# Kernel optimization log

Measured on AMD Instinct MI355X. Metric: run time of the kernel, lower is better.

Reference implementation:

```python
import jax, jax.numpy as jnp
import numpy as np

K = 32   # tokens_per_obs (hard-coded in module)
V = 512  # vocab_size

def setup_inputs() -> dict:
    key = jax.random.key(0)
    ks = jax.random.split(key, 10)
    s = 0.02  # small init scale for numerical sanity
    return {
        "x": jax.random.normal(ks[0], (4096, 512), jnp.float32),
        "enc_w1": jax.random.normal(ks[1], (512, 512), jnp.float32) * s,
        "enc_b1": jnp.zeros((512,), jnp.float32),
        "enc_w2": jax.random.normal(ks[2], (512, 16384), jnp.float32) * s,
        "enc_b2": jnp.zeros((16384,), jnp.float32),
        "codebook": jax.random.uniform(ks[3], (16384, 256), jnp.float32, -1.0 / V, 1.0 / V),
        "dec_w1": jax.random.normal(ks[4], (256, 512), jnp.float32) * s,
        "dec_b1": jnp.zeros((512,), jnp.float32),
        "dec_w2": jax.random.normal(ks[5], (512, 512), jnp.float32) * s,
        "dec_b2": jnp.zeros((512,), jnp.float32),
    }

def reference(x, enc_w1, enc_b1, enc_w2, enc_b2, codebook,
              dec_w1, dec_b1, dec_w2, dec_b2):
    b = x.shape[0]
    # encoder MLP -> logits z of shape (b, K*V)
    h = jax.nn.relu(x @ enc_w1 + enc_b1)
    z = h @ enc_w2 + enc_b2
    zl = z.reshape(b, K, V)                      # (b, K, V) per-block logits
    # categorical sample per token block
    tokens = jax.random.categorical(jax.random.key(1), zl, axis=-1)  # (b, K) int
    p = jax.nn.softmax(zl, axis=-1).reshape(b, K * V)
    oh = jax.nn.one_hot(tokens, V, dtype=p.dtype).reshape(b, K * V)
    # straight-through: forward value == one-hot, gradient flows through p
    st = p + jax.lax.stop_gradient(oh - p)
    z_q = st @ codebook                          # (b, embed_dim) = sum of K code rows
    # decoder MLP -> reconstruction
    rec = jax.nn.relu(z_q @ dec_w1 + dec_b1) @ dec_w2 + dec_b2
    return z, z_q, rec
```

## Files before the change

### kernel.cpp

```cpp
#include <hip/hip_runtime.h>
#include <hip/hip_bf16.h>
#include <math.h>
#include <stdint.h>


#define BATCH 4096
#define KTOK  32
#define VOCAB 512
#define DMODEL 512
#define ZDIM  16384
#define EDIM  256
#define MARGIN 0.03125f

typedef __attribute__((ext_vector_type(8))) short short8v;
typedef __attribute__((ext_vector_type(4))) float f32x4;

__device__ __forceinline__ uint32_t rotl32(uint32_t v, int r) {
    return (v << r) | (v >> (32 - r));
}

__device__ __forceinline__ void threefry2x32(uint32_t k0, uint32_t k1,
                                             uint32_t x0, uint32_t x1,
                                             uint32_t& y0, uint32_t& y1) {
    uint32_t ks0 = k0, ks1 = k1, ks2 = k0 ^ k1 ^ 0x1BD11BDAu;
    x0 += ks0; x1 += ks1;
#define TFR(r) { x0 += x1; x1 = rotl32(x1, r); x1 ^= x0; }
    TFR(13) TFR(15) TFR(26) TFR(6)
    x0 += ks1; x1 += ks2 + 1u;
    TFR(17) TFR(29) TFR(16) TFR(24)
    x0 += ks2; x1 += ks0 + 2u;
    TFR(13) TFR(15) TFR(26) TFR(6)
    x0 += ks0; x1 += ks1 + 3u;
    TFR(17) TFR(29) TFR(16) TFR(24)
    x0 += ks1; x1 += ks2 + 4u;
    TFR(13) TFR(15) TFR(26) TFR(6)
    x0 += ks2; x1 += ks0 + 5u;
#undef TFR
    y0 = x0; y1 = x1;
}

__device__ __forceinline__ float jax_gumbel(uint64_t e) {
    const float TINY = 1.17549435e-38f;
    uint32_t y0, y1;
    threefry2x32(0u, 1u, (uint32_t)(e >> 32), (uint32_t)(e & 0xffffffffull), y0, y1);
    uint32_t bits = y0 ^ y1;
    float u = __uint_as_float(0x3f800000u | (bits >> 9)) - 1.0f;
    u = u * 1.0f + TINY;
    u = fmaxf(TINY, u);
    return -logf(-logf(u));
}

__device__ __forceinline__ float fast_gumbel(uint32_t e32) {
    const float TINY = 1.17549435e-38f;
    const float LN2 = 0.69314718056f;
    uint32_t y0, y1;
    threefry2x32(0u, 1u, 0u, e32, y0, y1);
    uint32_t bits = y0 ^ y1;
    float f = __uint_as_float(0x3f800000u | (bits >> 9));
    float u = f - 1.0f;
    float d = 2.0f - f;
    u = fmaxf(u, TINY);
    float e_hw = -LN2 * __builtin_amdgcn_logf(u);
    float e_poly = d * fmaf(d, fmaf(d, 0.33333333f, 0.5f), 1.0f);
    float e = (d < 0.002f) ? e_poly : e_hw;
    return -LN2 * __builtin_amdgcn_logf(e);
}

__device__ __forceinline__ unsigned short f32_to_bf16_rne(float f) {
    uint32_t u = __float_as_uint(f);
    uint32_t r = (u + 0x7fffu + ((u >> 16) & 1u)) >> 16;
    return (unsigned short)r;
}

template<bool RELU>
__global__ __launch_bounds__(256)
void gemm_f32_64(const float* __restrict__ A, const float* __restrict__ B,
                 const float* __restrict__ bias, float* __restrict__ C,
                 int M, int N, int K) {
    constexpr int BK = 16;
    __shared__ __align__(16) float As[BK][68];
    __shared__ __align__(16) float Bs[BK][68];

    const int tid = threadIdx.x;
    const int tx = tid % 16;
    const int ty = tid / 16;
    const int brow = blockIdx.y * 64;
    const int bcol = blockIdx.x * 64;

    float acc[4][4] = {};

    for (int k0 = 0; k0 < K; k0 += BK) {
        {
            int r = tid >> 2, c4 = tid & 3;
            float4 v = *(const float4*)&A[(size_t)(brow + r) * K + k0 + c4 * 4];
            As[c4 * 4 + 0][r] = v.x;
            As[c4 * 4 + 1][r] = v.y;
            As[c4 * 4 + 2][r] = v.z;
            As[c4 * 4 + 3][r] = v.w;
        }
        {
            int r = tid >> 4, c4 = tid & 15;
            *(float4*)&Bs[r][c4 * 4] = *(const float4*)&B[(size_t)(k0 + r) * N + bcol + c4 * 4];
        }
        __syncthreads();

#pragma unroll
        for (int kk = 0; kk < BK; ++kk) {
            float a[4], b[4];
            *(float4*)&a[0] = *(const float4*)&As[kk][ty * 4];
            *(float4*)&b[0] = *(const float4*)&Bs[kk][tx * 4];
#pragma unroll
            for (int i = 0; i < 4; ++i)
#pragma unroll
                for (int j = 0; j < 4; ++j)
                    acc[i][j] = fmaf(a[i], b[j], acc[i][j]);
        }
        __syncthreads();
    }

#pragma unroll
    for (int i = 0; i < 4; ++i) {
        int row = brow + ty * 4 + i;
        int col = bcol + tx * 4;
        float4 v;
        v.x = acc[i][0] + bias[col + 0];
        v.y = acc[i][1] + bias[col + 1];
        v.z = acc[i][2] + bias[col + 2];
        v.w = acc[i][3] + bias[col + 3];
        if (RELU) {
            v.x = fmaxf(v.x, 0.0f); v.y = fmaxf(v.y, 0.0f);
            v.z = fmaxf(v.z, 0.0f); v.w = fmaxf(v.w, 0.0f);
        }
        *(float4*)&C[(size_t)row * N + col] = v;
    }
}

template<bool RELU>
__global__ __launch_bounds__(256)
void gemm_f32(const float* __restrict__ A, const float* __restrict__ B,
              const float* __restrict__ bias, float* __restrict__ C,
              int M, int N, int K) {
    constexpr int BM = 128, BN = 128, BK = 16, TM = 8, TN = 8;
    __shared__ __align__(16) float As[BK][BM + 4];
    __shared__ __align__(16) float Bs[BK][BN + 4];

    const int tid = threadIdx.x;
    const int tx = tid % (BN / TN);
    const int ty = tid / (BN / TN);
    const int brow = blockIdx.y * BM;
    const int bcol = blockIdx.x * BN;

    float acc[TM][TN] = {};

    for (int k0 = 0; k0 < K; k0 += BK) {
#pragma unroll
        for (int f = tid; f < BM * BK / 4; f += 256) {
            int r = f / (BK / 4);
            int c4 = f % (BK / 4);
            float4 v = *(const float4*)&A[(size_t)(brow + r) * K + k0 + c4 * 4];
            As[c4 * 4 + 0][r] = v.x;
            As[c4 * 4 + 1][r] = v.y;
            As[c4 * 4 + 2][r] = v.z;
            As[c4 * 4 + 3][r] = v.w;
        }
#pragma unroll
        for (int f = tid; f < BK * BN / 4; f += 256) {
            int r = f / (BN / 4);
            int c4 = f % (BN / 4);
            *(float4*)&Bs[r][c4 * 4] = *(const float4*)&B[(size_t)(k0 + r) * N + bcol + c4 * 4];
        }
        __syncthreads();

#pragma unroll
        for (int kk = 0; kk < BK; ++kk) {
            float a[TM], b[TN];
            *(float4*)&a[0] = *(const float4*)&As[kk][ty * TM];
            *(float4*)&a[4] = *(const float4*)&As[kk][ty * TM + 4];
            *(float4*)&b[0] = *(const float4*)&Bs[kk][tx * TN];
            *(float4*)&b[4] = *(const float4*)&Bs[kk][tx * TN + 4];
#pragma unroll
            for (int i = 0; i < TM; ++i)
#pragma unroll
                for (int j = 0; j < TN; ++j)
                    acc[i][j] = fmaf(a[i], b[j], acc[i][j]);
        }
        __syncthreads();
    }

#pragma unroll
    for (int i = 0; i < TM; ++i) {
        int row = brow + ty * TM + i;
#pragma unroll
        for (int j = 0; j < TN; j += 4) {
            int col = bcol + tx * TN + j;
            float4 v;
            v.x = acc[i][j + 0] + bias[col + 0];
            v.y = acc[i][j + 1] + bias[col + 1];
            v.z = acc[i][j + 2] + bias[col + 2];
            v.w = acc[i][j + 3] + bias[col + 3];
            if (RELU) {
                v.x = fmaxf(v.x, 0.0f); v.y = fmaxf(v.y, 0.0f);
                v.z = fmaxf(v.z, 0.0f); v.w = fmaxf(v.w, 0.0f);
            }
            *(float4*)&C[(size_t)row * N + col] = v;
        }
    }
}

__global__ __launch_bounds__(256)
void cvt_to_bf16(const float* __restrict__ src, unsigned short* __restrict__ dst,
                 int n) {
    int i = blockIdx.x * 256 + threadIdx.x;
    if (i * 4 < n) {
        float4 v = *(const float4*)&src[i * 4];
        ushort4 o;
        o.x = f32_to_bf16_rne(v.x);
        o.y = f32_to_bf16_rne(v.y);
        o.z = f32_to_bf16_rne(v.z);
        o.w = f32_to_bf16_rne(v.w);
        *(ushort4*)&dst[i * 4] = o;
    }
}

__global__ __launch_bounds__(256)
void transpose_w2(const float* __restrict__ src, unsigned short* __restrict__ dstb,
                  float* __restrict__ dstf, int R, int C, int writeF) {
    __shared__ float tile[32][33];
    const int c0 = blockIdx.x * 32, r0 = blockIdx.y * 32;
    const int tx = threadIdx.x % 32, ty = threadIdx.x / 32;
#pragma unroll
    for (int i = ty; i < 32; i += 8)
        tile[i][tx] = src[(size_t)(r0 + i) * C + c0 + tx];
    __syncthreads();
#pragma unroll
    for (int i = ty; i < 32; i += 8) {
        float v = tile[tx][i];
        size_t o = (size_t)(c0 + i) * R + r0 + tx;
        dstb[o] = f32_to_bf16_rne(v);
        if (writeF) dstf[o] = v;
    }
}

__global__ __launch_bounds__(256)
void gemm_mfma_bf16(const unsigned short* __restrict__ A,
                    const unsigned short* __restrict__ Bt,
                    const float* __restrict__ bias,
                    float* __restrict__ C,
                    int M, int N, int K) {
    constexpr int BM = 128, BN = 128, BK = 32;
    __shared__ unsigned short As[BM * BK];
    __shared__ unsigned short Bs[BN * BK];

    const int nwg = gridDim.x * gridDim.y;
    const int lid = blockIdx.y * gridDim.x + blockIdx.x;
    const int cpx = nwg >> 3;
    const int swz = (lid & 7) * cpx + (lid >> 3);
    const int bx = swz % gridDim.x;
    const int by = swz / gridDim.x;

    const int tid = threadIdx.x;
    const int wid = tid >> 6;
    const int lane = tid & 63;
    const int wr = wid >> 1, wc = wid & 1;
    const int l15 = lane & 15, lq = lane >> 4;
    const int brow = by * BM;
    const int bcol = bx * BN;

    const int g1 = tid;
    const int g2 = tid + 256;
    const size_t a1 = (size_t)(brow + (g1 >> 2)) * K + (g1 & 3) * 8;
    const size_t a2 = (size_t)(brow + (g2 >> 2)) * K + (g2 & 3) * 8;
    const size_t b1 = (size_t)(bcol + (g1 >> 2)) * K + (g1 & 3) * 8;
    const size_t b2 = (size_t)(bcol + (g2 >> 2)) * K + (g2 & 3) * 8;
    unsigned short* as_base1 = As + (size_t)wid * 64 * 8;
    unsigned short* as_base2 = As + (size_t)(256 + wid * 64) * 8;
    unsigned short* bs_base1 = Bs + (size_t)wid * 64 * 8;
    unsigned short* bs_base2 = Bs + (size_t)(256 + wid * 64) * 8;

    f32x4 acc[4][4];
#pragma unroll
    for (int m = 0; m < 4; ++m)
#pragma unroll
        for (int n = 0; n < 4; ++n) acc[m][n] = (f32x4){0.f, 0.f, 0.f, 0.f};

    for (int k0 = 0; k0 < K; k0 += BK) {
        __builtin_amdgcn_global_load_lds(
            (const __attribute__((address_space(1))) unsigned int*)(A + a1 + k0),
            (__attribute__((address_space(3))) unsigned int*)as_base1, 16, 0, 0);
        __builtin_amdgcn_global_load_lds(
            (const __attribute__((address_space(1))) unsigned int*)(A + a2 + k0),
            (__attribute__((address_space(3))) unsigned int*)as_base2, 16, 0, 0);
        __builtin_amdgcn_global_load_lds(
            (const __attribute__((address_space(1))) unsigned int*)(Bt + b1 + k0),
            (__attribute__((address_space(3))) unsigned int*)bs_base1, 16, 0, 0);
        __builtin_amdgcn_global_load_lds(
            (const __attribute__((address_space(1))) unsigned int*)(Bt + b2 + k0),
            (__attribute__((address_space(3))) unsigned int*)bs_base2, 16, 0, 0);
        __syncthreads();

        short8v af[4], bf[4];
#pragma unroll
        for (int m = 0; m < 4; ++m)
            af[m] = *(const short8v*)&As[(wr * 64 + m * 16 + l15) * BK + lq * 8];
#pragma unroll
        for (int n = 0; n < 4; ++n)
            bf[n] = *(const short8v*)&Bs[(wc * 64 + n * 16 + l15) * BK + lq * 8];
#pragma unroll
        for (int m = 0; m < 4; ++m)
#pragma unroll
            for (int n = 0; n < 4; ++n)
                acc[m][n] = __builtin_amdgcn_mfma_f32_16x16x32_bf16(
                    af[m], bf[n], acc[m][n], 0, 0, 0);
        __syncthreads();
    }

#pragma unroll
    for (int m = 0; m < 4; ++m) {
#pragma unroll
        for (int n = 0; n < 4; ++n) {
            int col = bcol + wc * 64 + n * 16 + l15;
            float bv = bias[col];
#pragma unroll
            for (int r = 0; r < 4; ++r) {
                int row = brow + wr * 64 + m * 16 + lq * 4 + r;
                C[(size_t)row * N + col] = acc[m][n][r] + bv;
            }
        }
    }
}

__global__ __launch_bounds__(256)
void sample_tokens_gap(const float* __restrict__ z, int* __restrict__ tokens,
                       float* __restrict__ s1v, int* __restrict__ amb,
                       int* __restrict__ ambCount) {
    const int wave = threadIdx.x >> 6;
    const int lane = threadIdx.x & 63;
    const uint32_t t = blockIdx.x * 4 + wave;
    const float* zr = z + (size_t)t * VOCAB;

    float s1 = -INFINITY, s2 = -INFINITY;
    int v1 = 0;
#pragma unroll
    for (int half = 0; half < 2; ++half) {
        int e0 = half * 256 + lane * 4;
        float4 zv = *(const float4*)&zr[e0];
        float zs[4] = {zv.x, zv.y, zv.z, zv.w};
#pragma unroll
        for (int j = 0; j < 4; ++j) {
            int v = e0 + j;
            float s = zs[j] + fast_gumbel(t * (uint32_t)VOCAB + v);
            if (s > s1 || (s == s1 && v < v1)) { s2 = s1; s1 = s; v1 = v; }
            else if (s > s2) s2 = s;
        }
    }
#pragma unroll
    for (int off = 32; off > 0; off >>= 1) {
        float os1 = __shfl_down(s1, off);
        int ov1 = __shfl_down(v1, off);
        float os2 = __shfl_down(s2, off);
        if (os1 > s1 || (os1 == s1 && ov1 < v1)) {
            s2 = fmaxf(s1, os2); s1 = os1; v1 = ov1;
        } else {
            s2 = fmaxf(os1, s2);
        }
    }
    if (lane == 0) {
        tokens[t] = v1;
        s1v[t] = s1;
        if (s1 - s2 < MARGIN) {
            int idx = atomicAdd(ambCount, 1);
            amb[idx] = (int)t;
        }
    }
}

__global__ __launch_bounds__(64)
void refine_tokens2(const float* __restrict__ z, const float* __restrict__ h,
                    const float* __restrict__ w2t, const float* __restrict__ eb2,
                    const int* __restrict__ amb, const int* __restrict__ ambCount,
                    const float* __restrict__ s1v, int* __restrict__ tok) {
    __shared__ float hrow[DMODEL];
    __shared__ int candv[64];
    const int cnt = *ambCount;
    const int lane = threadIdx.x;

    for (int i = blockIdx.x; i < cnt; i += gridDim.x) {
        const int t = amb[i];
        const int b = t >> 5;
        const int kb = t & 31;
        const float* zr = z + (size_t)t * VOCAB;
        const float s1 = s1v[t];

        {
            float4 hv0 = *(const float4*)&h[(size_t)b * DMODEL + lane * 8];
            float4 hv1 = *(const float4*)&h[(size_t)b * DMODEL + lane * 8 + 4];
            *(float4*)&hrow[lane * 8] = hv0;
            *(float4*)&hrow[lane * 8 + 4] = hv1;
        }

        int base = 0;
#pragma unroll
        for (int half = 0; half < 2; ++half) {
            int e0 = half * 256 + lane * 4;
            float4 zv = *(const float4*)&zr[e0];
            float zs[4] = {zv.x, zv.y, zv.z, zv.w};
#pragma unroll
            for (int j = 0; j < 4; ++j) {
                int v = e0 + j;
                float s = zs[j] + fast_gumbel((uint32_t)t * VOCAB + v);
                bool pred = (s >= s1 - MARGIN);
                unsigned long long mask = __ballot(pred);
                if (pred) {
                    int slot = base + __popcll(mask & ((1ull << lane) - 1ull));
                    if (slot < 64) candv[slot] = v;
                }
                base += __popcll(mask);
            }
        }
        __syncthreads();
        const int ncand = base < 64 ? base : 64;

        float bestE = -INFINITY;
        int bestV = VOCAB;
        if (lane < ncand) {
            const int v = candv[lane];
            const int n = kb * VOCAB + v;
            const float* wr_ = w2t + (size_t)n * DMODEL;
            float acc = 0.f;
#pragma unroll 8
            for (int k = 0; k < DMODEL; ++k)
                acc = fmaf(hrow[k], wr_[k], acc);
            bestE = acc + eb2[n] + jax_gumbel((uint64_t)t * VOCAB + v);
            bestV = v;
        }
#pragma unroll
        for (int off = 32; off > 0; off >>= 1) {
            float oe = __shfl_down(bestE, off);
            int ov = __shfl_down(bestV, off);
            if (oe > bestE || (oe == bestE && ov < bestV)) { bestE = oe; bestV = ov; }
        }
        if (lane == 0) tok[t] = bestV;
        __syncthreads();
    }
}

__global__ __launch_bounds__(64)
void refine_tokens(const float* __restrict__ z, const float* __restrict__ h,
                   const float* __restrict__ w2, const float* __restrict__ eb2,
                   const int* __restrict__ amb, const int* __restrict__ ambCount,
                   const float* __restrict__ s1v, int* __restrict__ tok) {
    const int cnt = *ambCount;
    const int lane = threadIdx.x;
    for (int i = blockIdx.x; i < cnt; i += gridDim.x) {
        const int t = amb[i];
        const int b = t >> 5;
        const int kb = t & 31;
        const float* zr = z + (size_t)t * VOCAB;
        const float s1 = s1v[t];
        float bestE = -INFINITY;
        int bestV = VOCAB;
#pragma unroll 1
        for (int r = 0; r < 8; ++r) {
            const int v = r * 64 + lane;
            const float g = jax_gumbel((uint64_t)t * VOCAB + v);
            const float sbf = zr[v] + g;
            float ex = -INFINITY;
            if (sbf >= s1 - MARGIN) {
                const float* hr = h + (size_t)b * DMODEL;
                const float* wcol = w2 + (size_t)(kb * VOCAB + v);
                float acc = 0.f;
#pragma unroll 8
                for (int k = 0; k < DMODEL; ++k)
                    acc = fmaf(hr[k], wcol[(size_t)k * ZDIM], acc);
                ex = acc + eb2[kb * VOCAB + v] + g;
            }
            if (ex > bestE || (ex == bestE && v < bestV)) { bestE = ex; bestV = v; }
        }
#pragma unroll
        for (int off = 32; off > 0; off >>= 1) {
            float oe = __shfl_down(bestE, off);
            int ov = __shfl_down(bestV, off);
            if (oe > bestE || (oe == bestE && ov < bestV)) { bestE = oe; bestV = ov; }
        }
        if (lane == 0) tok[t] = bestV;
    }
}

__global__ __launch_bounds__(256)
void sample_tokens_simple(const float* __restrict__ z, int* __restrict__ tokens) {
    const int wave = threadIdx.x >> 6;
    const int lane = threadIdx.x & 63;
    const size_t t = (size_t)blockIdx.x * 4 + wave;
    const float* zr = z + t * VOCAB;
    float zv[8];
    *(float4*)&zv[0] = *(const float4*)&zr[lane * 8];
    *(float4*)&zv[4] = *(const float4*)&zr[lane * 8 + 4];
    const uint64_t ebase = t * (uint64_t)VOCAB + (uint64_t)lane * 8;
    float best = -INFINITY;
    int bestv = 0;
#pragma unroll
    for (int j = 0; j < 8; ++j) {
        float g = jax_gumbel(ebase + j);
        float s = zv[j] + g;
        int v = lane * 8 + j;
        if (s > best || (s == best && v < bestv)) { best = s; bestv = v; }
    }
#pragma unroll
    for (int off = 32; off > 0; off >>= 1) {
        float ob = __shfl_down(best, off);
        int ov = __shfl_down(bestv, off);
        if (ob > best || (ob == best && ov < bestv)) { best = ob; bestv = ov; }
    }
    if (lane == 0) tokens[t] = bestv;
}

__global__ __launch_bounds__(64)
void zero_count(int* p) { if (threadIdx.x == 0) *p = 0; }

__global__ __launch_bounds__(256)
void gather_zq(const int* __restrict__ tokens, const float* __restrict__ codebook,
               float* __restrict__ zq) {
    const int b = blockIdx.x;
    const int d = threadIdx.x;
    float s = 0.0f;
#pragma unroll
    for (int k = 0; k < KTOK; ++k) {
        int tok = tokens[b * KTOK + k];
        s += codebook[(size_t)(k * VOCAB + tok) * EDIM + d];
    }
    zq[(size_t)b * EDIM + d] = s;
}

extern "C" void kernel_launch(void* const* d_in, const int* in_sizes, int n_in,
                              void* d_out, int out_size, void* d_ws, size_t ws_size,
                              hipStream_t stream) {
    const float* x   = (const float*)d_in[0];
    const float* ew1 = (const float*)d_in[1];
    const float* eb1 = (const float*)d_in[2];
    const float* ew2 = (const float*)d_in[3];
    const float* eb2 = (const float*)d_in[4];
    const float* cb  = (const float*)d_in[5];
    const float* dw1 = (const float*)d_in[6];
    const float* db1 = (const float*)d_in[7];
    const float* dw2 = (const float*)d_in[8];
    const float* db2 = (const float*)d_in[9];

    float* out = (float*)d_out;
    float* z   = out;
    float* zq  = out + (size_t)BATCH * ZDIM;
    float* rec = zq + (size_t)BATCH * EDIM;

    char* ws = (char*)d_ws;
    float* h    = (float*)(ws);
    float* h2   = (float*)(ws + 8388608);
    unsigned short* hb   = (unsigned short*)(ws + 16777216);
    unsigned short* w2bt = (unsigned short*)(ws + 20971520);
    float* w2t  = (float*)(ws + 37748736);
    const size_t WS_NEED1 = 39321856;
    const size_t WS_NEED2 = 37748736 + 33554432 + 1572864 + 256;
    const bool fast  = ws_size >= WS_NEED1;
    const bool fast2 = ws_size >= WS_NEED2;
    char* tail = fast2 ? (ws + 37748736 + 33554432) : (ws + 37748736);
    int*   tok  = (int*)(tail);
    float* s1v  = (float*)(tail + 524288);
    int*   amb  = (int*)(tail + 1048576);
    int*   cnt  = (int*)(tail + 1572864);

    dim3 blk(256);

    gemm_f32_64<true ><<<dim3(DMODEL / 64, BATCH / 64), blk, 0, stream>>>(
        x, ew1, eb1, h, BATCH, DMODEL, DMODEL);

    if (fast) {
        cvt_to_bf16<<<dim3(BATCH * DMODEL / 4 / 256), blk, 0, stream>>>(
            h, hb, BATCH * DMODEL);
        transpose_w2<<<dim3(ZDIM / 32, DMODEL / 32), blk, 0, stream>>>(
            ew2, w2bt, w2t, DMODEL, ZDIM, fast2 ? 1 : 0);
        gemm_mfma_bf16<<<dim3(ZDIM / 128, BATCH / 128), blk, 0, stream>>>(
            hb, w2bt, eb2, z, BATCH, ZDIM, DMODEL);
        zero_count<<<dim3(1), dim3(64), 0, stream>>>(cnt);
        sample_tokens_gap<<<dim3(BATCH * KTOK / 4), blk, 0, stream>>>(
            z, tok, s1v, amb, cnt);
        if (fast2) {
            refine_tokens2<<<dim3(4096), dim3(64), 0, stream>>>(
                z, h, w2t, eb2, amb, cnt, s1v, tok);
        } else {
            refine_tokens<<<dim3(2048), dim3(64), 0, stream>>>(
                z, h, ew2, eb2, amb, cnt, s1v, tok);
        }
    } else {
        gemm_f32<false><<<dim3(ZDIM / 128, BATCH / 128), blk, 0, stream>>>(
            h, ew2, eb2, z, BATCH, ZDIM, DMODEL);
        sample_tokens_simple<<<dim3(BATCH * KTOK / 4), blk, 0, stream>>>(z, tok);
    }

    gather_zq<<<dim3(BATCH), blk, 0, stream>>>(tok, cb, zq);

    gemm_f32_64<true ><<<dim3(DMODEL / 64, BATCH / 64), blk, 0, stream>>>(
        zq, dw1, db1, h2, BATCH, DMODEL, EDIM);
    gemm_f32_64<false><<<dim3(DMODEL / 64, BATCH / 64), blk, 0, stream>>>(
        h2, dw2, db2, rec, BATCH, DMODEL, DMODEL);
}
```

Measured before the change: 448.7 us.

## Fuse encoder GEMM with Gumbel top-2 sampling in one kernel

Replaces the separate bf16 MFMA GEMM and the sampling kernel with one kernel. Each block computes a 64x512 tile of z, which covers one vocab block per row, and adds Gumbel noise in the epilogue. It then does the top-2 reduction through shuffles and LDS, writing tokens and ambiguity flags directly. This removes the second full read of the 256MB z tensor. The cost is a different tile shape (512-thread blocks, 2x8 accumulators) and heavy threefry work in the GEMM epilogue, which may lower occupancy.

```diff
diff --git a/kernel.cpp b/kernel.cpp
--- a/kernel.cpp
+++ b/kernel.cpp
@@ -15,16 +15,12 @@
 typedef __attribute__((ext_vector_type(8))) short short8v;
 typedef __attribute__((ext_vector_type(4))) float f32x4;
 
-__device__ __forceinline__ uint32_t rotl32(uint32_t v, int r) {
-    return (v << r) | (v >> (32 - r));
-}
-
 __device__ __forceinline__ void threefry2x32(uint32_t k0, uint32_t k1,
                                              uint32_t x0, uint32_t x1,
                                              uint32_t& y0, uint32_t& y1) {
     uint32_t ks0 = k0, ks1 = k1, ks2 = k0 ^ k1 ^ 0x1BD11BDAu;
     x0 += ks0; x1 += ks1;
-#define TFR(r) { x0 += x1; x1 = rotl32(x1, r); x1 ^= x0; }
+#define TFR(r) { x0 += x1; x1 = __builtin_rotateleft32(x1, r); x1 ^= x0; }
     TFR(13) TFR(15) TFR(26) TFR(6)
     x0 += ks1; x1 += ks2 + 1u;
     TFR(17) TFR(29) TFR(16) TFR(24)
@@ -72,6 +68,28 @@
     return (unsigned short)r;
 }
 
+__device__ __forceinline__ void top2_push(float& s1, float& s2, int& v1,
+                                          float s, int v) {
+    if (s > s1 || (s == s1 && v < v1)) { s2 = s1; s1 = s; v1 = v; }
+    else s2 = fmaxf(s2, s);
+}
+__device__ __forceinline__ void top2_merge(float& s1, float& s2, int& v1,
+                                           float os1, float os2, int ov1) {
+    if (os1 > s1 || (os1 == s1 && ov1 < v1)) {
+        s2 = fmaxf(s1, os2);
+        s1 = os1; v1 = ov1;
+    } else {
+        s2 = fmaxf(s2, os1);
+    }
+}
+
+__device__ __forceinline__ void gload16(const unsigned short* src,
+                                        unsigned short* lds_base) {
+    __builtin_amdgcn_global_load_lds(
+        (const __attribute__((address_space(1))) unsigned int*)src,
+        (__attribute__((address_space(3))) unsigned int*)lds_base, 16, 0, 0);
+}
+
 template<bool RELU>
 __global__ __launch_bounds__(256)
 void gemm_f32_64(const float* __restrict__ A, const float* __restrict__ B,
@@ -241,133 +259,128 @@
     }
 }
 
-__global__ __launch_bounds__(256)
-void gemm_mfma_bf16(const unsigned short* __restrict__ A,
-                    const unsigned short* __restrict__ Bt,
-                    const float* __restrict__ bias,
-                    float* __restrict__ C,
-                    int M, int N, int K) {
-    constexpr int BM = 128, BN = 128, BK = 32;
-    __shared__ unsigned short As[BM * BK];
-    __shared__ unsigned short Bs[BN * BK];
-
-    const int nwg = gridDim.x * gridDim.y;
-    const int lid = blockIdx.y * gridDim.x + blockIdx.x;
-    const int cpx = nwg >> 3;
-    const int swz = (lid & 7) * cpx + (lid >> 3);
-    const int bx = swz % gridDim.x;
-    const int by = swz / gridDim.x;
+__global__ __launch_bounds__(512, 4)
+void gemm_fused_sample(const unsigned short* __restrict__ A,
+                       const unsigned short* __restrict__ Bt,
+                       const float* __restrict__ bias,
+                       float* __restrict__ C,
+                       int* __restrict__ tokens, float* __restrict__ s1v,
+                       int* __restrict__ amb, int* __restrict__ ambCount) {
+    __shared__ unsigned short As[4 * 64 * 8];
+    __shared__ unsigned short Bs[4 * 512 * 8];
+    __shared__ float redS1[64][4];
+    __shared__ float redS2[64][4];
+    __shared__ int   redV[64][4];
+
+    const int lid = blockIdx.x;
+    const int swz = (lid & 7) * 256 + (lid >> 3);
+    const int bx = swz >> 6;
+    const int by = swz & 63;
 
     const int tid = threadIdx.x;
     const int wid = tid >> 6;
     const int lane = tid & 63;
-    const int wr = wid >> 1, wc = wid & 1;
+    const int wr2 = wid >> 2, wc = wid & 3;
     const int l15 = lane & 15, lq = lane >> 4;
-    const int brow = by * BM;
-    const int bcol = bx * BN;
-
-    const int g1 = tid;
-    const int g2 = tid + 256;
-    const size_t a1 = (size_t)(brow + (g1 >> 2)) * K + (g1 & 3) * 8;
-    const size_t a2 = (size_t)(brow + (g2 >> 2)) * K + (g2 & 3) * 8;
-    const size_t b1 = (size_t)(bcol + (g1 >> 2)) * K + (g1 & 3) * 8;
-    const size_t b2 = (size_t)(bcol + (g2 >> 2)) * K + (g2 & 3) * 8;
-    unsigned short* as_base1 = As + (size_t)wid * 64 * 8;
-    unsigned short* as_base2 = As + (size_t)(256 + wid * 64) * 8;
-    unsigned short* bs_base1 = Bs + (size_t)wid * 64 * 8;
-    unsigned short* bs_base2 = Bs + (size_t)(256 + wid * 64) * 8;
-
-    f32x4 acc[4][4];
-#pragma unroll
-    for (int m = 0; m < 4; ++m)
-#pragma unroll
-        for (int n = 0; n < 4; ++n) acc[m][n] = (f32x4){0.f, 0.f, 0.f, 0.f};
-
-    for (int k0 = 0; k0 < K; k0 += BK) {
-        __builtin_amdgcn_global_load_lds(
-            (const __attribute__((address_space(1))) unsigned int*)(A + a1 + k0),
-            (__attribute__((address_space(3))) unsigned int*)as_base1, 16, 0, 0);
-        __builtin_amdgcn_global_load_lds(
-            (const __attribute__((address_space(1))) unsigned int*)(A + a2 + k0),
-            (__attribute__((address_space(3))) unsigned int*)as_base2, 16, 0, 0);
-        __builtin_amdgcn_global_load_lds(
-            (const __attribute__((address_space(1))) unsigned int*)(Bt + b1 + k0),
-            (__attribute__((address_space(3))) unsigned int*)bs_base1, 16, 0, 0);
-        __builtin_amdgcn_global_load_lds(
-            (const __attribute__((address_space(1))) unsigned int*)(Bt + b2 + k0),
-            (__attribute__((address_space(3))) unsigned int*)bs_base2, 16, 0, 0);
-        __syncthreads();
-
-        short8v af[4], bf[4];
-#pragma unroll
-        for (int m = 0; m < 4; ++m)
-            af[m] = *(const short8v*)&As[(wr * 64 + m * 16 + l15) * BK + lq * 8];
-#pragma unroll
-        for (int n = 0; n < 4; ++n)
-            bf[n] = *(const short8v*)&Bs[(wc * 64 + n * 16 + l15) * BK + lq * 8];
-#pragma unroll
-        for (int m = 0; m < 4; ++m)
-#pragma unroll
-            for (int n = 0; n < 4; ++n)
+    const int brow = by * 64;
+    const int bcol = bx * 512;
+
+    const unsigned short* aSrc = A + (size_t)(brow + lane) * DMODEL;
+    const unsigned short* bSrc = Bt + (size_t)(bcol + wid * 64 + lane) * DMODEL;
+
+    f32x4 acc[2][8];
+#pragma unroll
+    for (int m = 0; m < 2; ++m)
+#pragma unroll
+        for (int n = 0; n < 8; ++n) acc[m][n] = (f32x4){0.f, 0.f, 0.f, 0.f};
+
+    for (int k0 = 0; k0 < DMODEL; k0 += 32) {
+        if (wid < 4)
+            gload16(aSrc + k0 + wid * 8, As + wid * 512);
+#pragma unroll
+        for (int kq = 0; kq < 4; ++kq)
+            gload16(bSrc + k0 + kq * 8, Bs + kq * 4096 + wid * 512);
+        __syncthreads();
+
+        short8v af[2], bf[8];
+#pragma unroll
+        for (int m = 0; m < 2; ++m)
+            af[m] = *(const short8v*)&As[lq * 512 + (wr2 * 32 + m * 16 + l15) * 8];
+#pragma unroll
+        for (int n = 0; n < 8; ++n)
+            bf[n] = *(const short8v*)&Bs[lq * 4096 + (wc * 128 + n * 16 + l15) * 8];
+#pragma unroll
+        for (int m = 0; m < 2; ++m)
+#pragma unroll
+            for (int n = 0; n < 8; ++n)
                 acc[m][n] = __builtin_amdgcn_mfma_f32_16x16x32_bf16(
                     af[m], bf[n], acc[m][n], 0, 0, 0);
         __syncthreads();
     }
 
-#pragma unroll
-    for (int m = 0; m < 4; ++m) {
-#pragma unroll
-        for (int n = 0; n < 4; ++n) {
-            int col = bcol + wc * 64 + n * 16 + l15;
-            float bv = bias[col];
+    float s1[2][4], s2[2][4];
+    int v1[2][4];
+#pragma unroll
+    for (int m = 0; m < 2; ++m)
+#pragma unroll
+        for (int r = 0; r < 4; ++r) {
+            s1[m][r] = -INFINITY; s2[m][r] = -INFINITY; v1[m][r] = VOCAB;
+        }
+
+#pragma unroll
+    for (int m = 0; m < 2; ++m) {
+#pragma unroll
+        for (int n = 0; n < 8; ++n) {
+            const int col = wc * 128 + n * 16 + l15;
+            const float bv = bias[bcol + col];
 #pragma unroll
             for (int r = 0; r < 4; ++r) {
-                int row = brow + wr * 64 + m * 16 + lq * 4 + r;
-                C[(size_t)row * N + col] = acc[m][n][r] + bv;
+                const int row = wr2 * 32 + m * 16 + lq * 4 + r;
+                const float val = acc[m][n][r] + bv;
+                C[(size_t)(brow + row) * ZDIM + bcol + col] = val;
+                const uint32_t t = (uint32_t)(brow + row) * KTOK + bx;
+                const float g = fast_gumbel(t * (uint32_t)VOCAB + (uint32_t)col);
+                top2_push(s1[m][r], s2[m][r], v1[m][r], val + g, col);
             }
         }
     }
-}
-
-__global__ __launch_bounds__(256)
-void sample_tokens_gap(const float* __restrict__ z, int* __restrict__ tokens,
-                       float* __restrict__ s1v, int* __restrict__ amb,
-                       int* __restrict__ ambCount) {
-    const int wave = threadIdx.x >> 6;
-    const int lane = threadIdx.x & 63;
-    const uint32_t t = blockIdx.x * 4 + wave;
-    const float* zr = z + (size_t)t * VOCAB;
-
-    float s1 = -INFINITY, s2 = -INFINITY;
-    int v1 = 0;
-#pragma unroll
-    for (int half = 0; half < 2; ++half) {
-        int e0 = half * 256 + lane * 4;
-        float4 zv = *(const float4*)&zr[e0];
-        float zs[4] = {zv.x, zv.y, zv.z, zv.w};
-#pragma unroll
-        for (int j = 0; j < 4; ++j) {
-            int v = e0 + j;
-            float s = zs[j] + fast_gumbel(t * (uint32_t)VOCAB + v);
-            if (s > s1 || (s == s1 && v < v1)) { s2 = s1; s1 = s; v1 = v; }
-            else if (s > s2) s2 = s;
-        }
-    }
-#pragma unroll
-    for (int off = 32; off > 0; off >>= 1) {
-        float os1 = __shfl_down(s1, off);
-        int ov1 = __shfl_down(v1, off);
-        float os2 = __shfl_down(s2, off);
-        if (os1 > s1 || (os1 == s1 && ov1 < v1)) {
-            s2 = fmaxf(s1, os2); s1 = os1; v1 = ov1;
-        } else {
-            s2 = fmaxf(os1, s2);
-        }
-    }
-    if (lane == 0) {
-        tokens[t] = v1;
-        s1v[t] = s1;
-        if (s1 - s2 < MARGIN) {
+
+#pragma unroll
+    for (int off = 1; off < 16; off <<= 1) {
+#pragma unroll
+        for (int m = 0; m < 2; ++m)
+#pragma unroll
+            for (int r = 0; r < 4; ++r) {
+                float os1 = __shfl_xor(s1[m][r], off);
+                float os2 = __shfl_xor(s2[m][r], off);
+                int   ov1 = __shfl_xor(v1[m][r], off);
+                top2_merge(s1[m][r], s2[m][r], v1[m][r], os1, os2, ov1);
+            }
+    }
+    if (l15 == 0) {
+#pragma unroll
+        for (int m = 0; m < 2; ++m)
+#pragma unroll
+            for (int r = 0; r < 4; ++r) {
+                const int row = wr2 * 32 + m * 16 + lq * 4 + r;
+                redS1[row][wc] = s1[m][r];
+                redS2[row][wc] = s2[m][r];
+                redV[row][wc]  = v1[m][r];
+            }
+    }
+    __syncthreads();
+
+    if (tid < 64) {
+        const int row = tid;
+        float S1 = -INFINITY, S2 = -INFINITY;
+        int V1 = VOCAB;
+#pragma unroll
+        for (int w = 0; w < 4; ++w)
+            top2_merge(S1, S2, V1, redS1[row][w], redS2[row][w], redV[row][w]);
+        const uint32_t t = (uint32_t)(brow + row) * KTOK + bx;
+        tokens[t] = V1;
+        s1v[t] = S1;
+        if (S1 - S2 < MARGIN) {
             int idx = atomicAdd(ambCount, 1);
             amb[idx] = (int)t;
         }
@@ -576,11 +589,9 @@
             h, hb, BATCH * DMODEL);
         transpose_w2<<<dim3(ZDIM / 32, DMODEL / 32), blk, 0, stream>>>(
             ew2, w2bt, w2t, DMODEL, ZDIM, fast2 ? 1 : 0);
-        gemm_mfma_bf16<<<dim3(ZDIM / 128, BATCH / 128), blk, 0, stream>>>(
-            hb, w2bt, eb2, z, BATCH, ZDIM, DMODEL);
         zero_count<<<dim3(1), dim3(64), 0, stream>>>(cnt);
-        sample_tokens_gap<<<dim3(BATCH * KTOK / 4), blk, 0, stream>>>(
-            z, tok, s1v, amb, cnt);
+        gemm_fused_sample<<<dim3(2048), dim3(512), 0, stream>>>(
+            hb, w2bt, eb2, z, tok, s1v, amb, cnt);
         if (fast2) {
             refine_tokens2<<<dim3(4096), dim3(64), 0, stream>>>(
                 z, h, w2t, eb2, amb, cnt, s1v, tok);
```

New measurement: 501.4 us. 1.12x slower.

## Fuse gumbel top-2 sampling into MFMA GEMM epilogue and bf16 cast into GEMM1

Applied to the files above, without the earlier changes.

The bf16 GEMM epilogue now adds the Gumbel noise and computes per-row top-2 partials over each 64-column slice. The partials are merged by a small kernel that compacts ambiguous tokens using a wave ballot and one atomic per wave. This avoids re-reading the 256MB logits tensor in a separate sampling pass. The first GEMM also writes a bf16 copy of h directly, which removes the conversion kernel. In exchange the GEMM epilogue carries much more ALU work from the hash and log evaluations, and the workspace requirement grows.

```diff
diff --git a/kernel.cpp b/kernel.cpp
--- a/kernel.cpp
+++ b/kernel.cpp
@@ -15,16 +15,12 @@
 typedef __attribute__((ext_vector_type(8))) short short8v;
 typedef __attribute__((ext_vector_type(4))) float f32x4;
 
-__device__ __forceinline__ uint32_t rotl32(uint32_t v, int r) {
-    return (v << r) | (v >> (32 - r));
-}
-
 __device__ __forceinline__ void threefry2x32(uint32_t k0, uint32_t k1,
                                              uint32_t x0, uint32_t x1,
                                              uint32_t& y0, uint32_t& y1) {
     uint32_t ks0 = k0, ks1 = k1, ks2 = k0 ^ k1 ^ 0x1BD11BDAu;
     x0 += ks0; x1 += ks1;
-#define TFR(r) { x0 += x1; x1 = rotl32(x1, r); x1 ^= x0; }
+#define TFR(r) { x0 += x1; x1 = __builtin_rotateleft32(x1, r); x1 ^= x0; }
     TFR(13) TFR(15) TFR(26) TFR(6)
     x0 += ks1; x1 += ks2 + 1u;
     TFR(17) TFR(29) TFR(16) TFR(24)
@@ -72,10 +68,33 @@
     return (unsigned short)r;
 }
 
+__device__ __forceinline__ void top2_push(float& s1, float& s2, int& v1,
+                                          float s, int v) {
+    if (s > s1 || (s == s1 && v < v1)) { s2 = s1; s1 = s; v1 = v; }
+    else s2 = fmaxf(s2, s);
+}
+__device__ __forceinline__ void top2_merge(float& s1, float& s2, int& v1,
+                                           float os1, float os2, int ov1) {
+    if (os1 > s1 || (os1 == s1 && ov1 < v1)) {
+        s2 = fmaxf(s1, os2);
+        s1 = os1; v1 = ov1;
+    } else {
+        s2 = fmaxf(s2, os1);
+    }
+}
+
+__device__ __forceinline__ void gload16(const unsigned short* src,
+                                        unsigned short* lds_base) {
+    __builtin_amdgcn_global_load_lds(
+        (const __attribute__((address_space(1))) unsigned int*)src,
+        (__attribute__((address_space(3))) unsigned int*)lds_base, 16, 0, 0);
+}
+
 template<bool RELU>
 __global__ __launch_bounds__(256)
 void gemm_f32_64(const float* __restrict__ A, const float* __restrict__ B,
                  const float* __restrict__ bias, float* __restrict__ C,
+                 unsigned short* __restrict__ Cb,
                  int M, int N, int K) {
     constexpr int BK = 16;
     __shared__ __align__(16) float As[BK][68];
@@ -132,6 +151,14 @@
             v.z = fmaxf(v.z, 0.0f); v.w = fmaxf(v.w, 0.0f);
         }
         *(float4*)&C[(size_t)row * N + col] = v;
+        if (Cb) {
+            ushort4 o;
+            o.x = f32_to_bf16_rne(v.x);
+            o.y = f32_to_bf16_rne(v.y);
+            o.z = f32_to_bf16_rne(v.z);
+            o.w = f32_to_bf16_rne(v.w);
+            *(ushort4*)&Cb[(size_t)row * N + col] = o;
+        }
     }
 }
 
@@ -208,21 +235,6 @@
 }
 
 __global__ __launch_bounds__(256)
-void cvt_to_bf16(const float* __restrict__ src, unsigned short* __restrict__ dst,
-                 int n) {
-    int i = blockIdx.x * 256 + threadIdx.x;
-    if (i * 4 < n) {
-        float4 v = *(const float4*)&src[i * 4];
-        ushort4 o;
-        o.x = f32_to_bf16_rne(v.x);
-        o.y = f32_to_bf16_rne(v.y);
-        o.z = f32_to_bf16_rne(v.z);
-        o.w = f32_to_bf16_rne(v.w);
-        *(ushort4*)&dst[i * 4] = o;
-    }
-}
-
-__global__ __launch_bounds__(256)
 void transpose_w2(const float* __restrict__ src, unsigned short* __restrict__ dstb,
                   float* __restrict__ dstf, int R, int C, int writeF) {
     __shared__ float tile[32][33];
@@ -242,11 +254,12 @@
 }
 
 __global__ __launch_bounds__(256)
-void gemm_mfma_bf16(const unsigned short* __restrict__ A,
-                    const unsigned short* __restrict__ Bt,
-                    const float* __restrict__ bias,
-                    float* __restrict__ C,
-                    int M, int N, int K) {
+void gemm_mfma_fused(const unsigned short* __restrict__ A,
+                     const unsigned short* __restrict__ Bt,
+                     const float* __restrict__ bias,
+                     float* __restrict__ C,
+                     float4* __restrict__ part,
+                     int M, int N, int K) {
     constexpr int BM = 128, BN = 128, BK = 32;
     __shared__ unsigned short As[BM * BK];
     __shared__ unsigned short Bs[BN * BK];
@@ -284,18 +297,10 @@
         for (int n = 0; n < 4; ++n) acc[m][n] = (f32x4){0.f, 0.f, 0.f, 0.f};
 
     for (int k0 = 0; k0 < K; k0 += BK) {
-        __builtin_amdgcn_global_load_lds(
-            (const __attribute__((address_space(1))) unsigned int*)(A + a1 + k0),
-            (__attribute__((address_space(3))) unsigned int*)as_base1, 16, 0, 0);
-        __builtin_amdgcn_global_load_lds(
-            (const __attribute__((address_space(1))) unsigned int*)(A + a2 + k0),
-            (__attribute__((address_space(3))) unsigned int*)as_base2, 16, 0, 0);
-        __builtin_amdgcn_global_load_lds(
-            (const __attribute__((address_space(1))) unsigned int*)(Bt + b1 + k0),
-            (__attribute__((address_space(3))) unsigned int*)bs_base1, 16, 0, 0);
-        __builtin_amdgcn_global_load_lds(
-            (const __attribute__((address_space(1))) unsigned int*)(Bt + b2 + k0),
-            (__attribute__((address_space(3))) unsigned int*)bs_base2, 16, 0, 0);
+        gload16(A + a1 + k0, as_base1);
+        gload16(A + a2 + k0, as_base2);
+        gload16(Bt + b1 + k0, bs_base1);
+        gload16(Bt + b2 + k0, bs_base2);
         __syncthreads();
 
         short8v af[4], bf[4];
@@ -314,63 +319,80 @@
         __syncthreads();
     }
 
+    const int kb = bcol >> 9;
+    const int hx = ((bcol & 511) >> 6) + wc;
+
 #pragma unroll
     for (int m = 0; m < 4; ++m) {
+        float s1[4], s2[4];
+        int v1[4];
+#pragma unroll
+        for (int r = 0; r < 4; ++r) {
+            s1[r] = -INFINITY; s2[r] = -INFINITY; v1[r] = VOCAB;
+        }
 #pragma unroll
         for (int n = 0; n < 4; ++n) {
-            int col = bcol + wc * 64 + n * 16 + l15;
-            float bv = bias[col];
+            const int col = bcol + wc * 64 + n * 16 + l15;
+            const int vglob = col & 511;
+            const float bv = bias[col];
 #pragma unroll
             for (int r = 0; r < 4; ++r) {
-                int row = brow + wr * 64 + m * 16 + lq * 4 + r;
-                C[(size_t)row * N + col] = acc[m][n][r] + bv;
+                const int row = brow + wr * 64 + m * 16 + lq * 4 + r;
+                const float val = acc[m][n][r] + bv;
+                C[(size_t)row * N + col] = val;
+                const uint32_t t = (uint32_t)row * KTOK + kb;
+                const float g = fast_gumbel(t * (uint32_t)VOCAB + (uint32_t)vglob);
+                top2_push(s1[r], s2[r], v1[r], val + g, vglob);
             }
         }
-    }
-}
-
-__global__ __launch_bounds__(256)
-void sample_tokens_gap(const float* __restrict__ z, int* __restrict__ tokens,
-                       float* __restrict__ s1v, int* __restrict__ amb,
-                       int* __restrict__ ambCount) {
-    const int wave = threadIdx.x >> 6;
+#pragma unroll
+        for (int off = 1; off < 16; off <<= 1) {
+#pragma unroll
+            for (int r = 0; r < 4; ++r) {
+                float os1 = __shfl_xor(s1[r], off);
+                float os2 = __shfl_xor(s2[r], off);
+                int   ov1 = __shfl_xor(v1[r], off);
+                top2_merge(s1[r], s2[r], v1[r], os1, os2, ov1);
+            }
+        }
+        if (l15 == 0) {
+#pragma unroll
+            for (int r = 0; r < 4; ++r) {
+                const int row = brow + wr * 64 + m * 16 + lq * 4 + r;
+                const uint32_t t = (uint32_t)row * KTOK + kb;
+                float4 p;
+                p.x = s1[r]; p.y = s2[r];
+                p.z = __int_as_float(v1[r]); p.w = 0.f;
+                part[(size_t)t * 8 + hx] = p;
+            }
+        }
+    }
+}
+
+__global__ __launch_bounds__(256)
+void merge_sample(const float4* __restrict__ part, int* __restrict__ tokens,
+                  float* __restrict__ s1v, int* __restrict__ amb,
+                  int* __restrict__ ambCount) {
+    const int t = blockIdx.x * 256 + threadIdx.x;
     const int lane = threadIdx.x & 63;
-    const uint32_t t = blockIdx.x * 4 + wave;
-    const float* zr = z + (size_t)t * VOCAB;
-
-    float s1 = -INFINITY, s2 = -INFINITY;
-    int v1 = 0;
-#pragma unroll
-    for (int half = 0; half < 2; ++half) {
-        int e0 = half * 256 + lane * 4;
-        float4 zv = *(const float4*)&zr[e0];
-        float zs[4] = {zv.x, zv.y, zv.z, zv.w};
-#pragma unroll
-        for (int j = 0; j < 4; ++j) {
-            int v = e0 + j;
-            float s = zs[j] + fast_gumbel(t * (uint32_t)VOCAB + v);
-            if (s > s1 || (s == s1 && v < v1)) { s2 = s1; s1 = s; v1 = v; }
-            else if (s > s2) s2 = s;
-        }
-    }
-#pragma unroll
-    for (int off = 32; off > 0; off >>= 1) {
-        float os1 = __shfl_down(s1, off);
-        int ov1 = __shfl_down(v1, off);
-        float os2 = __shfl_down(s2, off);
-        if (os1 > s1 || (os1 == s1 && ov1 < v1)) {
-            s2 = fmaxf(s1, os2); s1 = os1; v1 = ov1;
-        } else {
-            s2 = fmaxf(os1, s2);
-        }
-    }
-    if (lane == 0) {
-        tokens[t] = v1;
-        s1v[t] = s1;
-        if (s1 - s2 < MARGIN) {
-            int idx = atomicAdd(ambCount, 1);
-            amb[idx] = (int)t;
-        }
+    float S1 = -INFINITY, S2 = -INFINITY;
+    int V1 = VOCAB;
+#pragma unroll
+    for (int hx = 0; hx < 8; ++hx) {
+        float4 p = part[(size_t)t * 8 + hx];
+        top2_merge(S1, S2, V1, p.x, p.y, __float_as_int(p.z));
+    }
+    tokens[t] = V1;
+    s1v[t] = S1;
+    const bool pred = (S1 - S2 < MARGIN);
+    unsigned long long mask = __ballot(pred);
+    if (pred) {
+        const int leader = (int)__ffsll((long long)mask) - 1;
+        int base = 0;
+        if (lane == leader) base = atomicAdd(ambCount, __popcll(mask));
+        base = __shfl(base, leader);
+        const int slot = base + __popcll(mask & ((1ull << lane) - 1ull));
+        amb[slot] = t;
     }
 }
 
@@ -441,48 +463,6 @@
         }
         if (lane == 0) tok[t] = bestV;
         __syncthreads();
-    }
-}
-
-__global__ __launch_bounds__(64)
-void refine_tokens(const float* __restrict__ z, const float* __restrict__ h,
-                   const float* __restrict__ w2, const float* __restrict__ eb2,
-                   const int* __restrict__ amb, const int* __restrict__ ambCount,
-                   const float* __restrict__ s1v, int* __restrict__ tok) {
-    const int cnt = *ambCount;
-    const int lane = threadIdx.x;
-    for (int i = blockIdx.x; i < cnt; i += gridDim.x) {
-        const int t = amb[i];
-        const int b = t >> 5;
-        const int kb = t & 31;
-        const float* zr = z + (size_t)t * VOCAB;
-        const float s1 = s1v[t];
-        float bestE = -INFINITY;
-        int bestV = VOCAB;
-#pragma unroll 1
-        for (int r = 0; r < 8; ++r) {
-            const int v = r * 64 + lane;
-            const float g = jax_gumbel((uint64_t)t * VOCAB + v);
-            const float sbf = zr[v] + g;
-            float ex = -INFINITY;
-            if (sbf >= s1 - MARGIN) {
-                const float* hr = h + (size_t)b * DMODEL;
-                const float* wcol = w2 + (size_t)(kb * VOCAB + v);
-                float acc = 0.f;
-#pragma unroll 8
-                for (int k = 0; k < DMODEL; ++k)
-                    acc = fmaf(hr[k], wcol[(size_t)k * ZDIM], acc);
-                ex = acc + eb2[kb * VOCAB + v] + g;
-            }
-            if (ex > bestE || (ex == bestE && v < bestV)) { bestE = ex; bestV = v; }
-        }
-#pragma unroll
-        for (int off = 32; off > 0; off >>= 1) {
-            float oe = __shfl_down(bestE, off);
-            int ov = __shfl_down(bestV, off);
-            if (oe > bestE || (oe == bestE && ov < bestV)) { bestE = oe; bestV = ov; }
-        }
-        if (lane == 0) tok[t] = bestV;
     }
 }
 
@@ -556,11 +536,11 @@
     unsigned short* hb   = (unsigned short*)(ws + 16777216);
     unsigned short* w2bt = (unsigned short*)(ws + 20971520);
     float* w2t  = (float*)(ws + 37748736);
-    const size_t WS_NEED1 = 39321856;
-    const size_t WS_NEED2 = 37748736 + 33554432 + 1572864 + 256;
-    const bool fast  = ws_size >= WS_NEED1;
+    float4* part = (float4*)(ws + 71303168);
+    char* tail = ws + 88080384;
+    const size_t WS_NEED2 = 88080384 + 1572864 + 256;
     const bool fast2 = ws_size >= WS_NEED2;
-    char* tail = fast2 ? (ws + 37748736 + 33554432) : (ws + 37748736);
+    if (!fast2) tail = ws + 16777216;
     int*   tok  = (int*)(tail);
     float* s1v  = (float*)(tail + 524288);
     int*   amb  = (int*)(tail + 1048576);
@@ -569,25 +549,19 @@
     dim3 blk(256);
 
     gemm_f32_64<true ><<<dim3(DMODEL / 64, BATCH / 64), blk, 0, stream>>>(
-        x, ew1, eb1, h, BATCH, DMODEL, DMODEL);
-
-    if (fast) {
-        cvt_to_bf16<<<dim3(BATCH * DMODEL / 4 / 256), blk, 0, stream>>>(
-            h, hb, BATCH * DMODEL);
+        x, ew1, eb1, h, fast2 ? hb : (unsigned short*)nullptr,
+        BATCH, DMODEL, DMODEL);
+
+    if (fast2) {
         transpose_w2<<<dim3(ZDIM / 32, DMODEL / 32), blk, 0, stream>>>(
-            ew2, w2bt, w2t, DMODEL, ZDIM, fast2 ? 1 : 0);
-        gemm_mfma_bf16<<<dim3(ZDIM / 128, BATCH / 128), blk, 0, stream>>>(
-            hb, w2bt, eb2, z, BATCH, ZDIM, DMODEL);
+            ew2, w2bt, w2t, DMODEL, ZDIM, 1);
         zero_count<<<dim3(1), dim3(64), 0, stream>>>(cnt);
-        sample_tokens_gap<<<dim3(BATCH * KTOK / 4), blk, 0, stream>>>(
-            z, tok, s1v, amb, cnt);
-        if (fast2) {
-            refine_tokens2<<<dim3(4096), dim3(64), 0, stream>>>(
-                z, h, w2t, eb2, amb, cnt, s1v, tok);
-        } else {
-            refine_tokens<<<dim3(2048), dim3(64), 0, stream>>>(
-                z, h, ew2, eb2, amb, cnt, s1v, tok);
-        }
+        gemm_mfma_fused<<<dim3(ZDIM / 128, BATCH / 128), blk, 0, stream>>>(
+            hb, w2bt, eb2, z, part, BATCH, ZDIM, DMODEL);
+        merge_sample<<<dim3(BATCH * KTOK / 256), blk, 0, stream>>>(
+            part, tok, s1v, amb, cnt);
+        refine_tokens2<<<dim3(4096), dim3(64), 0, stream>>>(
+            z, h, w2t, eb2, amb, cnt, s1v, tok);
     } else {
         gemm_f32<false><<<dim3(ZDIM / 128, BATCH / 128), blk, 0, stream>>>(
             h, ew2, eb2, z, BATCH, ZDIM, DMODEL);
@@ -597,7 +571,7 @@
     gather_zq<<<dim3(BATCH), blk, 0, stream>>>(tok, cb, zq);
 
     gemm_f32_64<true ><<<dim3(DMODEL / 64, BATCH / 64), blk, 0, stream>>>(
-        zq, dw1, db1, h2, BATCH, DMODEL, EDIM);
+        zq, dw1, db1, h2, nullptr, BATCH, DMODEL, EDIM);
     gemm_f32_64<false><<<dim3(DMODEL / 64, BATCH / 64), blk, 0, stream>>>(
-        h2, dw2, db2, rec, BATCH, DMODEL, DMODEL);
-}
+        h2, dw2, db2, rec, nullptr, BATCH, DMODEL, DMODEL);
+}
```

Result: slower. 527.2 us (+17.5%).
